# Kernel tuning notes

Measured on AMD Instinct MI355X. Metric: run time of the kernel, lower is better.

The kernel has to match this reference:

```python
import jax, jax.numpy as jnp
import numpy as np

B, S, OD, E, H, L, HID = 8, 512, 128, 1024, 16, 8, 4096
HD = E // H


def _layer_norm(x, g, b, eps=1e-5):
    m = jnp.mean(x, axis=-1, keepdims=True)
    v = jnp.mean((x - m) ** 2, axis=-1, keepdims=True)
    return (x - m) * jax.lax.rsqrt(v + eps) * g + b


def _forward(x, W_obs, Wqkv, Wo, bo, ln1_g, ln1_b, W1, b1, W2, b2, ln2_g, ln2_b):
    # embed: z = pinv(W_obs) @ x  (W_obs: [OD, E] as in nn.Linear(E, OD).weight)
    inv = jnp.linalg.pinv(W_obs)                      # [E, OD]
    z = jnp.einsum('eo,bso->bse', inv, x)             # [B, S, E]
    # sinusoidal positional encoding (faithful to PositionalEncoding)
    pos = jnp.arange(S, dtype=z.dtype)[:, None]
    div = jnp.exp(jnp.arange(0, E, 2, dtype=z.dtype) * (-np.log(10000.0) / E))
    pe = jnp.zeros((S, E), z.dtype)
    pe = pe.at[:, 0::2].set(jnp.sin(pos * div)).at[:, 1::2].set(jnp.cos(pos * div))
    z = z + pe[None]
    scale = 1.0 / np.sqrt(HD)
    for l in range(L):
        # multi-head attention (explicit QK^T softmax AV, as in source)
        qkv = z @ Wqkv[l].T                           # [B, S, 3E]
        qkv = qkv.reshape(B, S, H, 3 * HD).transpose(0, 2, 1, 3)  # [B, H, S, 3*HD]
        q, k, v = jnp.split(qkv, 3, axis=-1)
        a = jax.nn.softmax(jnp.einsum('bhtd,bhud->bhtu', q, k) * scale, axis=-1)
        o = jnp.einsum('bhtu,bhud->bhtd', a, v)       # [B, H, S, HD]
        o = o.transpose(0, 2, 1, 3).reshape(B, S, E)
        attn = o @ Wo[l].T + bo[l]
        z = _layer_norm(z + attn, ln1_g[l], ln1_b[l])
        h = jax.nn.relu(z @ W1[l].T + b1[l]) @ W2[l].T + b2[l]
        z = _layer_norm(z + h, ln2_g[l], ln2_b[l])
    return z @ W_obs.T                                # x_hat: [B, S, OD]


def setup_inputs() -> dict:
    key = jax.random.key(0)
    ks = jax.random.split(key, 8)
    sc = 0.02
    return {
        'x': jax.random.normal(ks[0], (B, S, OD), jnp.float32),
        'W_obs': jax.random.normal(ks[1], (OD, E), jnp.float32) * sc,
        'Wqkv': jax.random.normal(ks[2], (L, 3 * E, E), jnp.float32) * sc,
        'Wo': jax.random.normal(ks[3], (L, E, E), jnp.float32) * sc,
        'bo': jnp.zeros((L, E), jnp.float32),
        'ln1_g': jnp.ones((L, E), jnp.float32),
        'ln1_b': jnp.zeros((L, E), jnp.float32),
        'W1': jax.random.normal(ks[4], (L, HID, E), jnp.float32) * sc,
        'b1': jnp.zeros((L, HID), jnp.float32),
        'W2': jax.random.normal(ks[5], (L, E, HID), jnp.float32) * sc,
        'b2': jnp.zeros((L, E), jnp.float32),
        'ln2_g': jnp.ones((L, E), jnp.float32),
        'ln2_b': jnp.zeros((L, E), jnp.float32),
    }


def reference(x, W_obs, Wqkv, Wo, bo, ln1_g, ln1_b, W1, b1, W2, b2, ln2_g, ln2_b):
    return _forward(x, W_obs, Wqkv, Wo, bo, ln1_g, ln1_b, W1, b1, W2, b2, ln2_g, ln2_b)
```

## Files before the change

kernel.cpp:

```cpp
#include <hip/hip_runtime.h>
#include <math.h>

typedef __attribute__((ext_vector_type(8))) short short8;
typedef __attribute__((ext_vector_type(4))) float f32x4;

__device__ __forceinline__ float bf2f(unsigned short u) {
    union { unsigned int i; float f; } x; x.i = ((unsigned int)u) << 16; return x.f;
}
__device__ __forceinline__ unsigned short f2bf(float f) {
    union { float f; unsigned int i; } x; x.f = f;
    unsigned int i = x.i;
    return (unsigned short)((i + 0x7fffu + ((i >> 16) & 1u)) >> 16);
}

__global__ __launch_bounds__(256) void sniff_dtype(const unsigned int* __restrict__ w,
                                                   int* __restrict__ flag)
{
    __shared__ int red[4];
    int t = threadIdx.x;
    int hits = 0;
    for (int u = 0; u < 16; ++u) {
        unsigned int word = w[t * 16 + u];
        unsigned int ex = (word >> 7) & 0xFFu;
        if (ex >= 100u && ex <= 126u) ++hits;
    }
#pragma unroll
    for (int off = 32; off >= 1; off >>= 1) hits += __shfl_xor(hits, off, 64);
    if ((t & 63) == 0) red[t >> 6] = hits;
    __syncthreads();
    if (t == 0) flag[0] = ((red[0] + red[1] + red[2] + red[3]) > 2048) ? 1 : 0;
}

__global__ __launch_bounds__(256) void cvt_in(const void* __restrict__ src, size_t elem_off,
                                              unsigned short* __restrict__ dst, int n,
                                              const int* __restrict__ flag)
{
    int i = (blockIdx.x * 256 + threadIdx.x) * 4;
    int m = *flag;
    if (i + 3 < n) {
        if (m) {
            const unsigned short* s = (const unsigned short*)src + elem_off + i;
            *(ushort4*)(dst + i) = *(const ushort4*)s;
        } else {
            const float* s = (const float*)src + elem_off + i;
            float4 v = *(const float4*)s;
            ushort4 o; o.x = f2bf(v.x); o.y = f2bf(v.y); o.z = f2bf(v.z); o.w = f2bf(v.w);
            *(ushort4*)(dst + i) = o;
        }
    } else {
        for (int u = i; u < n; ++u) {
            if (m) dst[u] = ((const unsigned short*)src)[elem_off + u];
            else   dst[u] = f2bf(((const float*)src)[elem_off + u]);
        }
    }
}

__global__ __launch_bounds__(256) void write_out(const unsigned short* __restrict__ src,
                                                 void* __restrict__ dst, int n,
                                                 const int* __restrict__ flag)
{
    int i = blockIdx.x * 256 + threadIdx.x;
    if (i >= n) return;
    unsigned short u = src[i];
    if ((u & 0x7F80u) == 0x7F80u) u = 0x447Au;
    if (*flag) ((unsigned short*)dst)[i] = u;
    else       ((float*)dst)[i] = bf2f(u);
}

__global__ __launch_bounds__(256) void gemm_bt(
    const unsigned short* __restrict__ A,
    const unsigned short* __restrict__ B,
    const unsigned short* __restrict__ bias,
    unsigned short* __restrict__ C,
    int M, int N, int K, int relu)
{
    __shared__ __align__(16) unsigned short As[128 * 32];
    __shared__ __align__(16) unsigned short Bs[128 * 32];
    const int t = threadIdx.x;
    const int lane = t & 63;
    const int w = t >> 6;
    const int la = lane & 15;
    const int quad = lane >> 4;
    const int m0 = blockIdx.y * 128;
    const int n0 = blockIdx.x * 128;
    const int wm = (w >> 1) * 64;
    const int wn = (w & 1) * 64;
    f32x4 acc[4][4];
#pragma unroll
    for (int i = 0; i < 4; ++i)
#pragma unroll
        for (int j = 0; j < 4; ++j) acc[i][j] = (f32x4){0.f, 0.f, 0.f, 0.f};

    const int row0 = t >> 2, seg0 = t & 3;
    const unsigned short* Ap = A + (size_t)(m0 + row0) * K + seg0 * 8;
    const unsigned short* Bp = B + (size_t)(n0 + row0) * K + seg0 * 8;

    for (int kt = 0; kt < K; kt += 32) {
        __syncthreads();
        {
            int4 va0 = *(const int4*)(Ap + kt);
            int4 va1 = *(const int4*)(Ap + (size_t)64 * K + kt);
            int4 vb0 = *(const int4*)(Bp + kt);
            int4 vb1 = *(const int4*)(Bp + (size_t)64 * K + kt);
            *(int4*)(As + row0 * 32 + seg0 * 8) = va0;
            *(int4*)(As + (row0 + 64) * 32 + seg0 * 8) = va1;
            *(int4*)(Bs + row0 * 32 + seg0 * 8) = vb0;
            *(int4*)(Bs + (row0 + 64) * 32 + seg0 * 8) = vb1;
        }
        __syncthreads();
        short8 af[4], bfr[4];
#pragma unroll
        for (int i = 0; i < 4; ++i)
            af[i] = *(const short8*)(As + (wm + i * 16 + la) * 32 + quad * 8);
#pragma unroll
        for (int j = 0; j < 4; ++j)
            bfr[j] = *(const short8*)(Bs + (wn + j * 16 + la) * 32 + quad * 8);
#pragma unroll
        for (int i = 0; i < 4; ++i)
#pragma unroll
            for (int j = 0; j < 4; ++j)
                acc[i][j] = __builtin_amdgcn_mfma_f32_16x16x32_bf16(af[i], bfr[j], acc[i][j], 0, 0, 0);
    }

#pragma unroll
    for (int j = 0; j < 4; ++j) {
        int n = n0 + wn + j * 16 + la;
        float bv = bias ? bf2f(bias[n]) : 0.0f;
#pragma unroll
        for (int i = 0; i < 4; ++i) {
#pragma unroll
            for (int r = 0; r < 4; ++r) {
                int m = m0 + wm + i * 16 + quad * 4 + r;
                float v = acc[i][j][r] + bv;
                if (relu) v = fmaxf(v, 0.0f);
                C[(size_t)m * N + n] = f2bf(v);
            }
        }
    }
}

__global__ __launch_bounds__(256, 3) void attn_kernel(
    const unsigned short* __restrict__ qkv,
    unsigned short* __restrict__ attn_out)
{
    __shared__ __align__(16) unsigned short Ks[128 * 72];
    __shared__ __align__(16) unsigned short Vt[64 * 136];
    __shared__ __align__(16) unsigned short Ps[4 * 16 * 136];

    const int t = threadIdx.x;
    const int lane = t & 63;
    const int w = t >> 6;
    const int la = lane & 15;
    const int quad = lane >> 4;

    int bid = blockIdx.y * 8 + blockIdx.x;
    int xcd = bid & 7, idx = bid >> 3;
    int bh = ((idx & 15) << 3) | xcd;
    int qt = idx >> 4;
    const int b = bh >> 4, h = bh & 15;
    const int q0 = qt * 64;
    const size_t rowbase = (size_t)b * 512;
    const int qoff = h * 192, koff = h * 192 + 64, voff = h * 192 + 128;

    short8 aq[2];
#pragma unroll
    for (int dc = 0; dc < 2; ++dc)
        aq[dc] = *(const short8*)(qkv + (rowbase + q0 + w * 16 + la) * 3072 + qoff + dc * 32 + quad * 8);

    unsigned short* PsW = Ps + w * (16 * 136);

    f32x4 oacc[4];
#pragma unroll
    for (int dt2 = 0; dt2 < 4; ++dt2) oacc[dt2] = (f32x4){0.f, 0.f, 0.f, 0.f};
    float mrun = -1e30f, lrun = 0.f;

#pragma unroll 1
    for (int c = 0; c < 4; ++c) {
        __syncthreads();
#pragma unroll
        for (int it = 0; it < 4; ++it) {
            int idx2 = it * 256 + t;
            int kk = idx2 >> 3, d8 = idx2 & 7;
            int4 v = *(const int4*)(qkv + (rowbase + c * 128 + kk) * 3072 + koff + d8 * 8);
            *(int4*)(Ks + kk * 72 + d8 * 8) = v;
        }
        {
            int d8 = t & 7, kq = t >> 3;
            int k0 = kq * 4;
            const unsigned short* vb = qkv + (rowbase + c * 128 + k0) * 3072 + voff + d8 * 8;
            union { int4 q; unsigned short s[8]; } a0, a1, a2, a3;
            a0.q = *(const int4*)(vb);
            a1.q = *(const int4*)(vb + 3072);
            a2.q = *(const int4*)(vb + 6144);
            a3.q = *(const int4*)(vb + 9216);
#pragma unroll
            for (int u = 0; u < 8; ++u) {
                ushort4 o; o.x = a0.s[u]; o.y = a1.s[u]; o.z = a2.s[u]; o.w = a3.s[u];
                *(ushort4*)(Vt + (d8 * 8 + u) * 136 + k0) = o;
            }
        }
        __syncthreads();

        f32x4 st[8];
#pragma unroll
        for (int kt2 = 0; kt2 < 8; ++kt2) {
            f32x4 acc = (f32x4){0.f, 0.f, 0.f, 0.f};
#pragma unroll
            for (int dc = 0; dc < 2; ++dc) {
                short8 af = *(const short8*)(Ks + (kt2 * 16 + la) * 72 + dc * 32 + quad * 8);
                acc = __builtin_amdgcn_mfma_f32_16x16x32_bf16(af, aq[dc], acc, 0, 0, 0);
            }
            st[kt2] = acc;
        }
        float pmax = -1e30f;
#pragma unroll
        for (int kt2 = 0; kt2 < 8; ++kt2) {
#pragma unroll
            for (int r = 0; r < 4; ++r) {
                st[kt2][r] *= 0.125f;
                pmax = fmaxf(pmax, st[kt2][r]);
            }
        }
        pmax = fmaxf(pmax, __shfl_xor(pmax, 16, 64));
        pmax = fmaxf(pmax, __shfl_xor(pmax, 32, 64));
        float mnew = fmaxf(mrun, pmax);
        float f = __expf(mrun - mnew);
        mrun = mnew;
        float psum = 0.f;
#pragma unroll
        for (int kt2 = 0; kt2 < 8; ++kt2) {
            float e0 = __expf(st[kt2][0] - mrun);
            float e1 = __expf(st[kt2][1] - mrun);
            float e2 = __expf(st[kt2][2] - mrun);
            float e3 = __expf(st[kt2][3] - mrun);
            psum += (e0 + e1) + (e2 + e3);
            ushort4 o; o.x = f2bf(e0); o.y = f2bf(e1); o.z = f2bf(e2); o.w = f2bf(e3);
            *(ushort4*)(PsW + la * 136 + kt2 * 16 + quad * 4) = o;
        }
        psum += __shfl_xor(psum, 16, 64);
        psum += __shfl_xor(psum, 32, 64);
        lrun = lrun * f + psum;
        float fr[4];
#pragma unroll
        for (int r = 0; r < 4; ++r) fr[r] = __shfl(f, quad * 4 + r, 64);
#pragma unroll
        for (int dt2 = 0; dt2 < 4; ++dt2)
#pragma unroll
            for (int r = 0; r < 4; ++r) oacc[dt2][r] *= fr[r];
        __syncthreads();
#pragma unroll
        for (int ks = 0; ks < 4; ++ks) {
            short8 pa = *(const short8*)(PsW + la * 136 + ks * 32 + quad * 8);
#pragma unroll
            for (int dt2 = 0; dt2 < 4; ++dt2) {
                short8 bv = *(const short8*)(Vt + (dt2 * 16 + la) * 136 + ks * 32 + quad * 8);
                oacc[dt2] = __builtin_amdgcn_mfma_f32_16x16x32_bf16(pa, bv, oacc[dt2], 0, 0, 0);
            }
        }
    }

    float linv = 1.0f / lrun;
    float lr[4];
#pragma unroll
    for (int r = 0; r < 4; ++r) lr[r] = __shfl(linv, quad * 4 + r, 64);
#pragma unroll
    for (int dt2 = 0; dt2 < 4; ++dt2) {
        int d = h * 64 + dt2 * 16 + la;
#pragma unroll
        for (int r = 0; r < 4; ++r) {
            int q = q0 + w * 16 + quad * 4 + r;
            attn_out[(rowbase + q) * 1024 + d] = f2bf(oacc[dt2][r] * lr[r]);
        }
    }
}

__global__ __launch_bounds__(256) void resid_ln(
    const unsigned short* __restrict__ z_in, const unsigned short* __restrict__ br,
    const unsigned short* __restrict__ g, const unsigned short* __restrict__ bb,
    unsigned short* __restrict__ z_out)
{
    __shared__ float red[4];
    const int m = blockIdx.x, t = threadIdx.x;
    float v[4];
#pragma unroll
    for (int u = 0; u < 4; ++u) {
        int e = t + u * 256;
        v[u] = bf2f(z_in[(size_t)m * 1024 + e]) + bf2f(br[(size_t)m * 1024 + e]);
    }
    float s = v[0] + v[1] + v[2] + v[3];
#pragma unroll
    for (int off = 32; off >= 1; off >>= 1) s += __shfl_xor(s, off, 64);
    if ((t & 63) == 0) red[t >> 6] = s;
    __syncthreads();
    float mean = (red[0] + red[1] + red[2] + red[3]) * (1.0f / 1024.0f);
    __syncthreads();
    float q = 0.f;
#pragma unroll
    for (int u = 0; u < 4; ++u) { float d = v[u] - mean; q += d * d; }
#pragma unroll
    for (int off = 32; off >= 1; off >>= 1) q += __shfl_xor(q, off, 64);
    if ((t & 63) == 0) red[t >> 6] = q;
    __syncthreads();
    float var = (red[0] + red[1] + red[2] + red[3]) * (1.0f / 1024.0f);
    float inv = rsqrtf(var + 1e-5f);
#pragma unroll
    for (int u = 0; u < 4; ++u) {
        int e = t + u * 256;
        float o = (v[u] - mean) * inv * bf2f(g[e]) + bf2f(bb[e]);
        z_out[(size_t)m * 1024 + e] = f2bf(o);
    }
}

__global__ void transpose_wobs(const unsigned short* __restrict__ W, unsigned short* __restrict__ WT)
{
    int idx = blockIdx.x * 256 + threadIdx.x;
    int o = idx >> 10, e = idx & 1023;
    WT[e * 128 + o] = W[idx];
}

__global__ void compute_G(const unsigned short* __restrict__ WT, float* __restrict__ G)
{
    int i = blockIdx.x, j = threadIdx.x;
    float s = 0.f;
    for (int e = 0; e < 1024; ++e)
        s += bf2f(WT[e * 128 + i]) * bf2f(WT[e * 128 + j]);
    G[i * 128 + j] = s;
}

__global__ __launch_bounds__(1024) void sweep_inv(const float* __restrict__ G, float* __restrict__ Gi)
{
    __shared__ float M[128 * 128];
    const int t = threadIdx.x;
    for (int i = t; i < 16384; i += 1024) M[i] = G[i];
    __syncthreads();
    const int j = t & 127;
    const int ib = t >> 7;
    for (int k = 0; k < 128; ++k) {
        float d = M[k * 128 + k];
        float p = 1.0f / d;
        float rj = M[k * 128 + j];
        float cv[16];
#pragma unroll
        for (int u = 0; u < 16; ++u)
            cv[u] = M[(ib + u * 8) * 128 + k];
        __syncthreads();
#pragma unroll
        for (int u = 0; u < 16; ++u) {
            int i = ib + u * 8;
            float nv;
            if (i == k && j == k)      nv = -p;
            else if (i == k)           nv = rj * p;
            else if (j == k)           nv = cv[u] * p;
            else                       nv = M[i * 128 + j] - cv[u] * rj * p;
            M[i * 128 + j] = nv;
        }
        __syncthreads();
    }
    for (int n = t; n < 16384; n += 1024) Gi[n] = -M[n];
}

__global__ void embed_y(const unsigned short* __restrict__ x, const float* __restrict__ Gi,
                        float* __restrict__ y)
{
    int m = blockIdx.x, t = threadIdx.x;
    float s = 0.f;
    for (int o = 0; o < 128; ++o)
        s += bf2f(x[(size_t)m * 128 + o]) * Gi[o * 128 + t];
    y[(size_t)m * 128 + t] = s;
}

__global__ __launch_bounds__(256) void embed_z(const float* __restrict__ y,
                                               const unsigned short* __restrict__ Wobs,
                                               unsigned short* __restrict__ zb)
{
    int m = blockIdx.x, t = threadIdx.x;
    int s = m & 511;
    float accv[4] = {0.f, 0.f, 0.f, 0.f};
    for (int o = 0; o < 128; ++o) {
        float yv = y[(size_t)m * 128 + o];
#pragma unroll
        for (int u = 0; u < 4; ++u) {
            int e = t + u * 256;
            accv[u] += yv * bf2f(Wobs[o * 1024 + e]);
        }
    }
#pragma unroll
    for (int u = 0; u < 4; ++u) {
        int e = t + u * 256;
        float freq = __expf(-0.008994473019508f * (float)(e & ~1));
        float ang = (float)s * freq;
        float pe = (e & 1) ? cosf(ang) : sinf(ang);
        float v = accv[u] + pe;
        zb[(size_t)m * 1024 + e] = f2bf(v);
    }
}

extern "C" void kernel_launch(void* const* d_in, const int* in_sizes, int n_in,
                              void* d_out, int out_size, void* d_ws, size_t ws_size,
                              hipStream_t stream)
{
    const void* x_raw     = d_in[0];
    const void* Wobs_raw  = d_in[1];
    const void* Wqkv_raw  = d_in[2];
    const void* Wo_raw    = d_in[3];
    const void* bo_raw    = d_in[4];
    const void* ln1g_raw  = d_in[5];
    const void* ln1b_raw  = d_in[6];
    const void* W1_raw    = d_in[7];
    const void* b1_raw    = d_in[8];
    const void* W2_raw    = d_in[9];
    const void* b2_raw    = d_in[10];
    const void* ln2g_raw  = d_in[11];
    const void* ln2b_raw  = d_in[12];

    char* ws = (char*)d_ws;
    constexpr size_t OFF_G    = 0;
    constexpr size_t OFF_GI   = OFF_G    + 65536;
    constexpr size_t OFF_Y    = OFF_GI   + 65536;
    constexpr size_t OFF_WT   = OFF_Y    + (size_t)4096 * 128 * 4;
    constexpr size_t OFF_ZB   = OFF_WT   + (size_t)1024 * 128 * 2;
    constexpr size_t OFF_QKV  = OFF_ZB   + (size_t)4096 * 1024 * 2;
    constexpr size_t OFF_ATT  = OFF_QKV  + (size_t)4096 * 3072 * 2;
    constexpr size_t OFF_FFN1 = OFF_QKV;
    constexpr size_t OFF_SCR  = OFF_ATT  + (size_t)4096 * 1024 * 2;
    constexpr size_t OFF_XBF  = OFF_SCR  + (size_t)4096 * 1024 * 2;
    constexpr size_t OFF_WOBS = OFF_XBF  + (size_t)524288 * 2;
    constexpr size_t OFF_CVT  = OFF_WOBS + (size_t)131072 * 2;
    constexpr size_t OFF_BO   = OFF_CVT  + (size_t)4096 * 1024 * 2;
    constexpr size_t OFF_B1   = OFF_BO   + 8192 * 2;
    constexpr size_t OFF_B2   = OFF_B1   + 32768 * 2;
    constexpr size_t OFF_L1G  = OFF_B2   + 8192 * 2;
    constexpr size_t OFF_L1B  = OFF_L1G  + 8192 * 2;
    constexpr size_t OFF_L2G  = OFF_L1B  + 8192 * 2;
    constexpr size_t OFF_L2B  = OFF_L2G  + 8192 * 2;
    constexpr size_t OFF_FLAG = OFF_L2B  + 8192 * 2;

    float* G             = (float*)(ws + OFF_G);
    float* Gi            = (float*)(ws + OFF_GI);
    float* y             = (float*)(ws + OFF_Y);
    unsigned short* WT   = (unsigned short*)(ws + OFF_WT);
    unsigned short* zb   = (unsigned short*)(ws + OFF_ZB);
    unsigned short* qkvb = (unsigned short*)(ws + OFF_QKV);
    unsigned short* attnb= (unsigned short*)(ws + OFF_ATT);
    unsigned short* ffn1 = (unsigned short*)(ws + OFF_FFN1);
    unsigned short* scr  = (unsigned short*)(ws + OFF_SCR);
    unsigned short* xbf  = (unsigned short*)(ws + OFF_XBF);
    unsigned short* wobs = (unsigned short*)(ws + OFF_WOBS);
    unsigned short* cvtb = (unsigned short*)(ws + OFF_CVT);
    unsigned short* boB  = (unsigned short*)(ws + OFF_BO);
    unsigned short* b1B  = (unsigned short*)(ws + OFF_B1);
    unsigned short* b2B  = (unsigned short*)(ws + OFF_B2);
    unsigned short* l1g  = (unsigned short*)(ws + OFF_L1G);
    unsigned short* l1b  = (unsigned short*)(ws + OFF_L1B);
    unsigned short* l2g  = (unsigned short*)(ws + OFF_L2G);
    unsigned short* l2b  = (unsigned short*)(ws + OFF_L2B);
    int* flag            = (int*)(ws + OFF_FLAG);

    sniff_dtype<<<1, 256, 0, stream>>>((const unsigned int*)Wobs_raw, flag);

    auto cvt = [&](const void* src, size_t off, unsigned short* dst, int n) {
        cvt_in<<<(n + 1023) / 1024, 256, 0, stream>>>(src, off, dst, n, flag);
    };

    cvt(x_raw, 0, xbf, 524288);
    cvt(Wobs_raw, 0, wobs, 131072);
    cvt(bo_raw, 0, boB, 8192);
    cvt(b1_raw, 0, b1B, 32768);
    cvt(b2_raw, 0, b2B, 8192);
    cvt(ln1g_raw, 0, l1g, 8192);
    cvt(ln1b_raw, 0, l1b, 8192);
    cvt(ln2g_raw, 0, l2g, 8192);
    cvt(ln2b_raw, 0, l2b, 8192);

    transpose_wobs<<<512, 256, 0, stream>>>(wobs, WT);
    compute_G<<<128, 128, 0, stream>>>(WT, G);
    sweep_inv<<<1, 1024, 0, stream>>>(G, Gi);
    embed_y<<<4096, 128, 0, stream>>>(xbf, Gi, y);
    embed_z<<<4096, 256, 0, stream>>>(y, wobs, zb);

    for (int l = 0; l < 8; ++l) {
        cvt(Wqkv_raw, (size_t)l * 3072 * 1024, cvtb, 3072 * 1024);
        gemm_bt<<<dim3(24, 32), 256, 0, stream>>>(zb, cvtb, nullptr, qkvb, 4096, 3072, 1024, 0);
        attn_kernel<<<dim3(8, 128), 256, 0, stream>>>(qkvb, attnb);
        cvt(Wo_raw, (size_t)l * 1024 * 1024, cvtb, 1024 * 1024);
        gemm_bt<<<dim3(8, 32), 256, 0, stream>>>(attnb, cvtb, boB + (size_t)l * 1024, scr, 4096, 1024, 1024, 0);
        resid_ln<<<4096, 256, 0, stream>>>(zb, scr, l1g + (size_t)l * 1024, l1b + (size_t)l * 1024, zb);
        cvt(W1_raw, (size_t)l * 4096 * 1024, cvtb, 4096 * 1024);
        gemm_bt<<<dim3(32, 32), 256, 0, stream>>>(zb, cvtb, b1B + (size_t)l * 4096, ffn1, 4096, 4096, 1024, 1);
        cvt(W2_raw, (size_t)l * 1024 * 4096, cvtb, 1024 * 4096);
        gemm_bt<<<dim3(8, 32), 256, 0, stream>>>(ffn1, cvtb, b2B + (size_t)l * 1024, scr, 4096, 1024, 4096, 0);
        resid_ln<<<4096, 256, 0, stream>>>(zb, scr, l2g + (size_t)l * 1024, l2b + (size_t)l * 1024, zb);
    }

    gemm_bt<<<dim3(1, 32), 256, 0, stream>>>(zb, wobs, nullptr, scr, 4096, 128, 1024, 0);
    write_out<<<(out_size + 255) / 256, 256, 0, stream>>>(scr, d_out, out_size, flag);
}
```

Baseline: 2.810 ms.

## Use direct global-to-LDS loads in GEMM and register-resident matrix inversion

The GEMM tile loads now go straight from global memory into shared memory through the global_load_lds builtin, so the data no longer passes through registers. The sweep-based Gram matrix inverse also changes: each thread keeps its 16 matrix entries in registers, and only the pivot row and pivot column are shared through small LDS buffers, replacing the full 64KB shared matrix. The aim is lower register and LDS traffic in the main GEMM and a cheaper inversion. The direct-to-LDS path depends on a layout where each lane writes a contiguous 16-byte slot, which carries correctness risk.

```diff
diff --git a/kernel.cpp b/kernel.cpp
--- a/kernel.cpp
+++ b/kernel.cpp
@@ -11,6 +11,14 @@
     union { float f; unsigned int i; } x; x.f = f;
     unsigned int i = x.i;
     return (unsigned short)((i + 0x7fffu + ((i >> 16) & 1u)) >> 16);
+}
+
+__device__ __forceinline__ void gload16(const unsigned short* g, unsigned short* l)
+{
+    __builtin_amdgcn_global_load_lds(
+        (__attribute__((address_space(1))) void*)(g),
+        (__attribute__((address_space(3))) void*)(l),
+        16, 0, 0);
 }
 
 __global__ __launch_bounds__(256) void sniff_dtype(const unsigned int* __restrict__ w,
@@ -94,19 +102,17 @@
     const int row0 = t >> 2, seg0 = t & 3;
     const unsigned short* Ap = A + (size_t)(m0 + row0) * K + seg0 * 8;
     const unsigned short* Bp = B + (size_t)(n0 + row0) * K + seg0 * 8;
+    unsigned short* lA0 = As + row0 * 32 + seg0 * 8;
+    unsigned short* lA1 = As + (row0 + 64) * 32 + seg0 * 8;
+    unsigned short* lB0 = Bs + row0 * 32 + seg0 * 8;
+    unsigned short* lB1 = Bs + (row0 + 64) * 32 + seg0 * 8;
 
     for (int kt = 0; kt < K; kt += 32) {
         __syncthreads();
-        {
-            int4 va0 = *(const int4*)(Ap + kt);
-            int4 va1 = *(const int4*)(Ap + (size_t)64 * K + kt);
-            int4 vb0 = *(const int4*)(Bp + kt);
-            int4 vb1 = *(const int4*)(Bp + (size_t)64 * K + kt);
-            *(int4*)(As + row0 * 32 + seg0 * 8) = va0;
-            *(int4*)(As + (row0 + 64) * 32 + seg0 * 8) = va1;
-            *(int4*)(Bs + row0 * 32 + seg0 * 8) = vb0;
-            *(int4*)(Bs + (row0 + 64) * 32 + seg0 * 8) = vb1;
-        }
+        gload16(Ap + kt, lA0);
+        gload16(Ap + (size_t)64 * K + kt, lA1);
+        gload16(Bp + kt, lB0);
+        gload16(Bp + (size_t)64 * K + kt, lB1);
         __syncthreads();
         short8 af[4], bfr[4];
 #pragma unroll
@@ -329,34 +335,46 @@
 
 __global__ __launch_bounds__(1024) void sweep_inv(const float* __restrict__ G, float* __restrict__ Gi)
 {
-    __shared__ float M[128 * 128];
+    __shared__ float rowbuf[128];
+    __shared__ float colbuf[128];
     const int t = threadIdx.x;
-    for (int i = t; i < 16384; i += 1024) M[i] = G[i];
-    __syncthreads();
     const int j = t & 127;
     const int ib = t >> 7;
-    for (int k = 0; k < 128; ++k) {
-        float d = M[k * 128 + k];
-        float p = 1.0f / d;
-        float rj = M[k * 128 + j];
-        float cv[16];
-#pragma unroll
-        for (int u = 0; u < 16; ++u)
-            cv[u] = M[(ib + u * 8) * 128 + k];
-        __syncthreads();
-#pragma unroll
-        for (int u = 0; u < 16; ++u) {
-            int i = ib + u * 8;
-            float nv;
-            if (i == k && j == k)      nv = -p;
-            else if (i == k)           nv = rj * p;
-            else if (j == k)           nv = cv[u] * p;
-            else                       nv = M[i * 128 + j] - cv[u] * rj * p;
-            M[i * 128 + j] = nv;
-        }
-        __syncthreads();
-    }
-    for (int n = t; n < 16384; n += 1024) Gi[n] = -M[n];
+    float vals[16];
+#pragma unroll
+    for (int u = 0; u < 16; ++u)
+        vals[u] = G[(ib + u * 8) * 128 + j];
+
+#pragma unroll
+    for (int ku = 0; ku < 16; ++ku) {
+        for (int kib = 0; kib < 8; ++kib) {
+            const int k = ku * 8 + kib;
+            if (ib == kib) rowbuf[j] = vals[ku];
+            if (j == k) {
+#pragma unroll
+                for (int u = 0; u < 16; ++u) colbuf[ib + u * 8] = vals[u];
+            }
+            __syncthreads();
+            float d = rowbuf[k];
+            float p = 1.0f / d;
+            float rj = rowbuf[j];
+#pragma unroll
+            for (int u = 0; u < 16; ++u) {
+                int i = ib + u * 8;
+                float cv = colbuf[i];
+                float nv;
+                if (i == k && j == k)      nv = -p;
+                else if (i == k)           nv = rj * p;
+                else if (j == k)           nv = cv * p;
+                else                       nv = vals[u] - cv * rj * p;
+                vals[u] = nv;
+            }
+            __syncthreads();
+        }
+    }
+#pragma unroll
+    for (int u = 0; u < 16; ++u)
+        Gi[(ib + u * 8) * 128 + j] = -vals[u];
 }
 
 __global__ void embed_y(const unsigned short* __restrict__ x, const float* __restrict__ Gi,
```

New measurement: 2.702 ms. 1.04x faster.
